# Performance work log

Hardware: AMD Instinct MI355X
Metric: run time of the kernel (lower is better)

The kernel has to match this reference:

```python
import jax, jax.numpy as jnp
import numpy as np

GH, GW = 64, 64     # patch grid
WH, WW = 8, 8       # window size
NH = 8              # num heads
EMB = 128
HD = EMB // NH      # head dim = 16
M = WH * WW         # tokens per window = 64


def _masks():
    # Faithful to the torch code: row_mask blocks cross-shift attention for the
    # last window-row; column_mask is its einops-rearranged counterpart.
    half = WH * (WW // 2)
    row = np.zeros((M, M), np.float32)
    row[-half:, :-half] = -np.inf
    row[:-half, -half:] = -np.inf
    r, c = M // WH, M // WW
    # '(r wh) (c ww) -> (wh r) (ww c)'
    col = row.reshape(r, WH, c, WW).transpose(1, 0, 3, 2).reshape(M, M)
    return jnp.asarray(row), jnp.asarray(col)


def _rel_idx():
    hh, ww_ = np.meshgrid(np.arange(WH), np.arange(WW), indexing='ij')
    coords = np.stack([hh.ravel(), ww_.ravel()], -1)        # (M, 2)
    rel = coords[:, None, :] - coords[None, :, :]           # (M, M, 2)
    return jnp.asarray(rel[..., 0] + WH - 1), jnp.asarray(rel[..., 1] + WW - 1)


def setup_inputs() -> dict:
    key = jax.random.key(0)
    ks = jax.random.split(key, 4)
    B, L = 32, GH * GW
    return {
        'x': jax.random.normal(ks[0], (B, L, EMB), jnp.float32),
        'w1': jax.random.normal(ks[1], (3 * EMB, EMB), jnp.float32) * 0.02,
        'b1': jnp.zeros((3 * EMB,), jnp.float32),
        'w2': jax.random.normal(ks[2], (EMB, EMB), jnp.float32) * 0.02,
        'b2': jnp.zeros((EMB,), jnp.float32),
        'rel_bias': jax.random.normal(ks[3], (2 * WH - 1, 2 * WW - 1), jnp.float32) * 0.02,
    }


def reference(x, w1, b1, w2, b2, rel_bias):
    B, L, C = x.shape
    qkv = x @ w1.T + b1                                   # (B, L, 3C)
    # 'b (h w) (c k) -> b h w c k'  (k=3 varies fastest within channel)
    qkv = qkv.reshape(B, GH, GW, C, 3)
    # cyclic shift by half window
    qkv = jnp.roll(qkv, (-WH // 2, -WW // 2), axis=(1, 2))
    # 'b (Hw wh) (Ww ww) (e H) k -> b H Hw Ww (wh ww) e k'  (head idx fastest in C)
    qkv = qkv.reshape(B, GH // WH, WH, GW // WW, WW, HD, NH, 3)
    qkv = jnp.transpose(qkv, (0, 6, 1, 3, 2, 4, 5, 7))    # b H Hw Ww wh ww e k
    qkv = qkv.reshape(B, NH, GH // WH, GW // WW, M, HD, 3)
    Q, K, V = qkv[..., 0], qkv[..., 1], qkv[..., 2]
    wei = jnp.einsum('bhijqe,bhijke->bhijqk', Q, K) / float(np.sqrt(HD))
    ih, iw = _rel_idx()
    wei = wei + rel_bias[ih, iw]                          # (M, M) bias broadcast
    row_mask, col_mask = _masks()
    wei = wei.at[:, :, -1, :].add(row_mask)               # last window-row
    wei = wei.at[:, :, :, -1].add(col_mask)               # last window-col
    attn = jax.nn.softmax(wei, axis=-1)
    out = jnp.einsum('bhijqk,bhijke->bhijqe', attn, V)    # b H Hw Ww M e
    # 'b H Hw Ww (wh ww) e -> b (Hw wh) (Ww ww) (H e)' then flatten spatial
    out = out.reshape(B, NH, GH // WH, GW // WW, WH, WW, HD)
    out = jnp.transpose(out, (0, 2, 4, 3, 5, 1, 6)).reshape(B, L, C)
    return out @ w2.T + b2
```

## Files before the change

kernel.cpp:

```cpp
#include <hip/hip_runtime.h>
#include <math.h>

typedef _Float16 h4  __attribute__((ext_vector_type(4)));
typedef _Float16 h8  __attribute__((ext_vector_type(8)));
typedef float    f4  __attribute__((ext_vector_type(4)));
typedef float    f32x4 __attribute__((ext_vector_type(4)));

#define W1_ELEMS (384*128)
#define W2_ELEMS (128*128)
#define LOG2E 1.44269504088896340736f

__global__ void cvt_weights(const float* __restrict__ w1, const float* __restrict__ w2,
                            _Float16* __restrict__ w1h, _Float16* __restrict__ w2h) {
    int i = blockIdx.x * 256 + threadIdx.x;
    if (i < W1_ELEMS) {
        int j = i >> 7, k = i & 127;
        int c = j / 3;
        int kind = j - 3 * c;
        int jp = kind * 128 + (c & 7) * 16 + (c >> 3);
        w1h[jp * 128 + k] = (_Float16)w1[i];
    }
    if (i < W2_ELEMS) w2h[i] = (_Float16)w2[i];
}

__global__ __launch_bounds__(512, 4)
void swin_fused(const float* __restrict__ x,
                const float* __restrict__ b1,
                const float* __restrict__ b2,
                const float* __restrict__ rel_bias,
                const _Float16* __restrict__ w1h,
                const _Float16* __restrict__ w2h,
                float* __restrict__ out)
{
    __shared__ _Float16 xh[64*136];
    __shared__ _Float16 QO[8*64*16];
    __shared__ _Float16 Kt[8*64*16];
    __shared__ _Float16 Vt[8*16*68];
    __shared__ _Float16 bm[64*68];

    const int tid  = threadIdx.x;
    const int lane = tid & 63;
    const int wv   = tid >> 6;
    const int quad = lane >> 4;
    const int l16  = lane & 15;
    const int s_lane = (l16 & 3) ^ ((l16 >> 2) & 3);
    const int swz    = (quad ^ s_lane) << 2;

    const int blk = blockIdx.x;
    const int b   = blk >> 6;
    const int Hw  = (blk >> 3) & 7;
    const int Ww  = blk & 7;

    {
        const int r0 = tid >> 5;
        const int c4 = tid & 31;
        #pragma unroll
        for (int it = 0; it < 4; ++it) {
            int t  = r0 + it*16;
            int gi = (Hw*8 + (t >> 3) + 4) & 63;
            int gj = (Ww*8 + (t & 7) + 4) & 63;
            f32x4 v = *(const f32x4*)(x + ((size_t)b*4096 + gi*64 + gj)*128 + c4*4);
            h4 hv;
            hv[0] = (_Float16)v[0]; hv[1] = (_Float16)v[1];
            hv[2] = (_Float16)v[2]; hv[3] = (_Float16)v[3];
            *(h4*)(&xh[t*136 + c4*4]) = hv;
        }
    }
    {
        const int rowm = (Hw == 7);
        const int colm = (Ww == 7);
        #pragma unroll
        for (int it = 0; it < 8; ++it) {
            int f = tid + it*512;
            int j = f >> 6, i = f & 63;
            int hi = i >> 3, wi = i & 7, hj = j >> 3, wj = j & 7;
            float v = rel_bias[(hi - hj + 7)*15 + (wi - wj + 7)] * LOG2E;
            if (rowm && ((i ^ j) & 32)) v = -INFINITY;
            if (colm && ((i ^ j) & 4))  v = -INFINITY;
            bm[i*68 + j] = (_Float16)v;
        }
    }

    float biasv[3][4];
    #pragma unroll
    for (int cc = 0; cc < 3; ++cc)
        #pragma unroll
        for (int r = 0; r < 4; ++r)
            biasv[cc][r] = b1[96*quad + 24*r + 3*wv + cc];

    __syncthreads();

    _Float16* Qh = &QO[wv*1024];
    _Float16* Kh = &Kt[wv*1024];

    {
        f4 acc[3][4];
        #pragma unroll
        for (int cc = 0; cc < 3; ++cc)
            #pragma unroll
            for (int tt = 0; tt < 4; ++tt)
                acc[cc][tt] = (f4){0.f,0.f,0.f,0.f};

        for (int kb = 0; kb < 4; ++kb) {
            h8 bfx[4];
            #pragma unroll
            for (int tt = 0; tt < 4; ++tt)
                bfx[tt] = *(const h8*)(&xh[(tt*16 + l16)*136 + kb*32 + quad*8]);
            #pragma unroll
            for (int cc = 0; cc < 3; ++cc) {
                h8 afw = *(const h8*)(w1h + (size_t)((cc*8 + wv)*16 + l16)*128 + kb*32 + quad*8);
                #pragma unroll
                for (int tt = 0; tt < 4; ++tt)
                    acc[cc][tt] = __builtin_amdgcn_mfma_f32_16x16x32_f16(afw, bfx[tt], acc[cc][tt], 0, 0, 0);
            }
        }

        const float qsc = 0.25f * LOG2E;
        #pragma unroll
        for (int tt = 0; tt < 4; ++tt) {
            int t = tt*16 + l16;
            h4 qv, kv;
            #pragma unroll
            for (int r = 0; r < 4; ++r) {
                qv[r] = (_Float16)((acc[0][tt][r] + biasv[0][r]) * qsc);
                kv[r] = (_Float16)( acc[1][tt][r] + biasv[1][r]);
            }
            *(h4*)(Qh + t*16 + swz) = qv;
            *(h4*)(Kh + t*16 + swz) = kv;
            #pragma unroll
            for (int r = 0; r < 4; ++r)
                Vt[(wv*16 + quad*4 + r)*68 + t] = (_Float16)(acc[2][tt][r] + biasv[2][r]);
        }
    }

    {
        const _Float16* Vh = &Vt[wv*16*68];

        h4 ak[4];
        #pragma unroll
        for (int mt = 0; mt < 4; ++mt)
            ak[mt] = *(const h4*)(Kh + (mt*16 + l16)*16 + swz);
        h4 av[4];
        #pragma unroll
        for (int kt = 0; kt < 4; ++kt)
            av[kt] = *(const h4*)(Vh + l16*68 + kt*16 + quad*4);

        for (int nt = 0; nt < 4; ++nt) {
            h4 bq = *(const h4*)(Qh + (nt*16 + l16)*16 + swz);

            f4 T[4];
            #pragma unroll
            for (int mt = 0; mt < 4; ++mt) {
                f4 z = {0.f,0.f,0.f,0.f};
                T[mt] = __builtin_amdgcn_mfma_f32_16x16x16f16(ak[mt], bq, z, 0, 0, 0);
            }
            #pragma unroll
            for (int mt = 0; mt < 4; ++mt) {
                h4 bmv = *(const h4*)(&bm[(nt*16 + l16)*68 + mt*16 + quad*4]);
                #pragma unroll
                for (int r = 0; r < 4; ++r)
                    T[mt][r] += (float)bmv[r];
            }

            float m = -INFINITY;
            #pragma unroll
            for (int mt = 0; mt < 4; ++mt)
                #pragma unroll
                for (int r = 0; r < 4; ++r) m = fmaxf(m, T[mt][r]);
            m = fmaxf(m, __shfl_xor(m, 16, 64));
            m = fmaxf(m, __shfl_xor(m, 32, 64));
            float s = 0.f;
            h4 P[4];
            #pragma unroll
            for (int mt = 0; mt < 4; ++mt)
                #pragma unroll
                for (int r = 0; r < 4; ++r) {
                    float p = __builtin_amdgcn_exp2f(T[mt][r] - m);
                    s += p;
                    P[mt][r] = (_Float16)p;
                }
            s += __shfl_xor(s, 16, 64);
            s += __shfl_xor(s, 32, 64);
            float rcp = 1.0f / s;

            f4 o = {0.f,0.f,0.f,0.f};
            #pragma unroll
            for (int kt = 0; kt < 4; ++kt)
                o = __builtin_amdgcn_mfma_f32_16x16x16f16(av[kt], P[kt], o, 0, 0, 0);
            h4 ov;
            #pragma unroll
            for (int r = 0; r < 4; ++r) ov[r] = (_Float16)(o[r] * rcp);
            *(h4*)(Qh + (nt*16 + l16)*16 + swz) = ov;
        }
    }
    __syncthreads();

    {
        const int o = wv*16 + l16;
        const int g0 = (quad & 1) * 2;
        const int off0 = ((g0    ) ^ s_lane) << 2;
        const int off1 = ((g0 + 1) ^ s_lane) << 2;

        f4 acc3[4] = {{0.f,0.f,0.f,0.f},{0.f,0.f,0.f,0.f},{0.f,0.f,0.f,0.f},{0.f,0.f,0.f,0.f}};
        for (int kb = 0; kb < 4; ++kb) {
            h8 bf = *(const h8*)(w2h + (size_t)o*128 + kb*32 + quad*8);
            int hh = kb*2 + (quad >> 1);
            #pragma unroll
            for (int mt = 0; mt < 4; ++mt) {
                const _Float16* Ob = &QO[hh*1024 + (mt*16 + l16)*16];
                h4 a0 = *(const h4*)(Ob + off0);
                h4 a1 = *(const h4*)(Ob + off1);
                h8 af = { a0[0], a0[1], a0[2], a0[3], a1[0], a1[1], a1[2], a1[3] };
                acc3[mt] = __builtin_amdgcn_mfma_f32_16x16x32_f16(af, bf, acc3[mt], 0, 0, 0);
            }
        }
        float bias = b2[o];
        #pragma unroll
        for (int mt = 0; mt < 4; ++mt) {
            #pragma unroll
            for (int r = 0; r < 4; ++r) {
                int t  = mt*16 + quad*4 + r;
                int gi = Hw*8 + (t >> 3);
                int gj = Ww*8 + (t & 7);
                out[((size_t)b*4096 + gi*64 + gj)*128 + o] = acc3[mt][r] + bias;
            }
        }
    }
}

extern "C" void kernel_launch(void* const* d_in, const int* in_sizes, int n_in,
                              void* d_out, int out_size, void* d_ws, size_t ws_size,
                              hipStream_t stream) {
    (void)in_sizes; (void)n_in; (void)out_size; (void)ws_size;
    const float* x  = (const float*)d_in[0];
    const float* w1 = (const float*)d_in[1];
    const float* b1 = (const float*)d_in[2];
    const float* w2 = (const float*)d_in[3];
    const float* b2 = (const float*)d_in[4];
    const float* rb = (const float*)d_in[5];

    _Float16* w1h = (_Float16*)d_ws;
    _Float16* w2h = (_Float16*)((char*)d_ws + (size_t)W1_ELEMS * sizeof(_Float16));
    float* outp = (float*)d_out;

    cvt_weights<<<(W1_ELEMS + 255)/256, 256, 0, stream>>>(w1, w2, w1h, w2h);
    swin_fused<<<32*64, 512, 0, stream>>>(x, b1, b2, rb, w1h, w2h, outp);
}
```

Measured before the change: 157.0 us.

## Keep Q/K/V in registers and precompute bias-mask tables in prep kernel

QKV projection results now feed attention straight from MFMA accumulators. V is computed transposed so its fragment layout matches the PV MFMA operand. This removes the Q/K/V shared-memory round trip and its swizzle, and shrinks LDS to two 64x136 buffers. The four bias/mask variants are precomputed once into a global fp16 table by the weight-conversion kernel, replacing per-block rel_bias gathers with global reads of that table. Attention output is written to a row-major LDS tile, and the output-projection operands are loaded once up front. The trade-offs are higher register pressure and bias reads that now come from global memory/cache.

```diff
diff --git a/kernel.cpp b/kernel.cpp
--- a/kernel.cpp
+++ b/kernel.cpp
@@ -8,10 +8,13 @@
 
 #define W1_ELEMS (384*128)
 #define W2_ELEMS (128*128)
+#define BM_ELEMS (4*64*64)
 #define LOG2E 1.44269504088896340736f
 
 __global__ void cvt_weights(const float* __restrict__ w1, const float* __restrict__ w2,
-                            _Float16* __restrict__ w1h, _Float16* __restrict__ w2h) {
+                            const float* __restrict__ rel_bias,
+                            _Float16* __restrict__ w1h, _Float16* __restrict__ w2h,
+                            _Float16* __restrict__ bmg) {
     int i = blockIdx.x * 256 + threadIdx.x;
     if (i < W1_ELEMS) {
         int j = i >> 7, k = i & 127;
@@ -21,30 +24,33 @@
         w1h[jp * 128 + k] = (_Float16)w1[i];
     }
     if (i < W2_ELEMS) w2h[i] = (_Float16)w2[i];
+    if (i < BM_ELEMS) {
+        int v = i >> 12, f = i & 4095;
+        int ti = f >> 6, tj = f & 63;
+        float val = rel_bias[((ti >> 3) - (tj >> 3) + 7) * 15 + ((ti & 7) - (tj & 7) + 7)] * LOG2E;
+        if ((v & 2) && ((ti ^ tj) & 32)) val = -INFINITY;
+        if ((v & 1) && ((ti ^ tj) & 4))  val = -INFINITY;
+        bmg[i] = (_Float16)val;
+    }
 }
 
 __global__ __launch_bounds__(512, 4)
 void swin_fused(const float* __restrict__ x,
                 const float* __restrict__ b1,
                 const float* __restrict__ b2,
-                const float* __restrict__ rel_bias,
                 const _Float16* __restrict__ w1h,
                 const _Float16* __restrict__ w2h,
+                const _Float16* __restrict__ bmg,
                 float* __restrict__ out)
 {
     __shared__ _Float16 xh[64*136];
-    __shared__ _Float16 QO[8*64*16];
-    __shared__ _Float16 Kt[8*64*16];
-    __shared__ _Float16 Vt[8*16*68];
-    __shared__ _Float16 bm[64*68];
+    __shared__ _Float16 Ob[64*136];
 
     const int tid  = threadIdx.x;
     const int lane = tid & 63;
     const int wv   = tid >> 6;
     const int quad = lane >> 4;
     const int l16  = lane & 15;
-    const int s_lane = (l16 & 3) ^ ((l16 >> 2) & 3);
-    const int swz    = (quad ^ s_lane) << 2;
 
     const int blk = blockIdx.x;
     const int b   = blk >> 6;
@@ -66,87 +72,62 @@
             *(h4*)(&xh[t*136 + c4*4]) = hv;
         }
     }
+
+    float bQ[4], bK[4];
+    #pragma unroll
+    for (int r = 0; r < 4; ++r) {
+        bQ[r] = b1[24*(quad*4 + r) + 3*wv + 0];
+        bK[r] = b1[24*(quad*4 + r) + 3*wv + 1];
+    }
+    const float bV = b1[24*l16 + 3*wv + 2];
+
+    __syncthreads();
+
+    f4 accQ[4], accK[4], accV[4];
+    #pragma unroll
+    for (int tt = 0; tt < 4; ++tt) {
+        accQ[tt] = (f4){0.f,0.f,0.f,0.f};
+        accK[tt] = (f4){0.f,0.f,0.f,0.f};
+        accV[tt] = (f4){0.f,0.f,0.f,0.f};
+    }
+    for (int kb = 0; kb < 4; ++kb) {
+        h8 bfx[4];
+        #pragma unroll
+        for (int tt = 0; tt < 4; ++tt)
+            bfx[tt] = *(const h8*)(&xh[(tt*16 + l16)*136 + kb*32 + quad*8]);
+        h8 aQ = *(const h8*)(w1h + (size_t)((0*8 + wv)*16 + l16)*128 + kb*32 + quad*8);
+        h8 aK = *(const h8*)(w1h + (size_t)((1*8 + wv)*16 + l16)*128 + kb*32 + quad*8);
+        h8 aV = *(const h8*)(w1h + (size_t)((2*8 + wv)*16 + l16)*128 + kb*32 + quad*8);
+        #pragma unroll
+        for (int tt = 0; tt < 4; ++tt) {
+            accQ[tt] = __builtin_amdgcn_mfma_f32_16x16x32_f16(aQ, bfx[tt], accQ[tt], 0, 0, 0);
+            accK[tt] = __builtin_amdgcn_mfma_f32_16x16x32_f16(aK, bfx[tt], accK[tt], 0, 0, 0);
+            accV[tt] = __builtin_amdgcn_mfma_f32_16x16x32_f16(bfx[tt], aV, accV[tt], 0, 0, 0);
+        }
+    }
+
     {
-        const int rowm = (Hw == 7);
-        const int colm = (Ww == 7);
-        #pragma unroll
-        for (int it = 0; it < 8; ++it) {
-            int f = tid + it*512;
-            int j = f >> 6, i = f & 63;
-            int hi = i >> 3, wi = i & 7, hj = j >> 3, wj = j & 7;
-            float v = rel_bias[(hi - hj + 7)*15 + (wi - wj + 7)] * LOG2E;
-            if (rowm && ((i ^ j) & 32)) v = -INFINITY;
-            if (colm && ((i ^ j) & 4))  v = -INFINITY;
-            bm[i*68 + j] = (_Float16)v;
-        }
-    }
-
-    float biasv[3][4];
-    #pragma unroll
-    for (int cc = 0; cc < 3; ++cc)
-        #pragma unroll
-        for (int r = 0; r < 4; ++r)
-            biasv[cc][r] = b1[96*quad + 24*r + 3*wv + cc];
-
-    __syncthreads();
-
-    _Float16* Qh = &QO[wv*1024];
-    _Float16* Kh = &Kt[wv*1024];
-
-    {
-        f4 acc[3][4];
-        #pragma unroll
-        for (int cc = 0; cc < 3; ++cc)
-            #pragma unroll
-            for (int tt = 0; tt < 4; ++tt)
-                acc[cc][tt] = (f4){0.f,0.f,0.f,0.f};
-
-        for (int kb = 0; kb < 4; ++kb) {
-            h8 bfx[4];
-            #pragma unroll
-            for (int tt = 0; tt < 4; ++tt)
-                bfx[tt] = *(const h8*)(&xh[(tt*16 + l16)*136 + kb*32 + quad*8]);
-            #pragma unroll
-            for (int cc = 0; cc < 3; ++cc) {
-                h8 afw = *(const h8*)(w1h + (size_t)((cc*8 + wv)*16 + l16)*128 + kb*32 + quad*8);
-                #pragma unroll
-                for (int tt = 0; tt < 4; ++tt)
-                    acc[cc][tt] = __builtin_amdgcn_mfma_f32_16x16x32_f16(afw, bfx[tt], acc[cc][tt], 0, 0, 0);
-            }
-        }
-
+        const _Float16* bmp = bmg + ((((Hw == 7) ? 2 : 0) | ((Ww == 7) ? 1 : 0)) << 12);
         const float qsc = 0.25f * LOG2E;
-        #pragma unroll
-        for (int tt = 0; tt < 4; ++tt) {
-            int t = tt*16 + l16;
-            h4 qv, kv;
-            #pragma unroll
-            for (int r = 0; r < 4; ++r) {
-                qv[r] = (_Float16)((acc[0][tt][r] + biasv[0][r]) * qsc);
-                kv[r] = (_Float16)( acc[1][tt][r] + biasv[1][r]);
-            }
-            *(h4*)(Qh + t*16 + swz) = qv;
-            *(h4*)(Kh + t*16 + swz) = kv;
+
+        h4 ak[4];
+        #pragma unroll
+        for (int mt = 0; mt < 4; ++mt)
             #pragma unroll
             for (int r = 0; r < 4; ++r)
-                Vt[(wv*16 + quad*4 + r)*68 + t] = (_Float16)(acc[2][tt][r] + biasv[2][r]);
-        }
-    }
-
-    {
-        const _Float16* Vh = &Vt[wv*16*68];
-
-        h4 ak[4];
-        #pragma unroll
-        for (int mt = 0; mt < 4; ++mt)
-            ak[mt] = *(const h4*)(Kh + (mt*16 + l16)*16 + swz);
+                ak[mt][r] = (_Float16)(accK[mt][r] + bK[r]);
         h4 av[4];
         #pragma unroll
         for (int kt = 0; kt < 4; ++kt)
-            av[kt] = *(const h4*)(Vh + l16*68 + kt*16 + quad*4);
+            #pragma unroll
+            for (int r = 0; r < 4; ++r)
+                av[kt][r] = (_Float16)(accV[kt][r] + bV);
 
         for (int nt = 0; nt < 4; ++nt) {
-            h4 bq = *(const h4*)(Qh + (nt*16 + l16)*16 + swz);
+            h4 bq;
+            #pragma unroll
+            for (int i = 0; i < 4; ++i)
+                bq[i] = (_Float16)((accQ[nt][i] + bQ[i]) * qsc);
 
             f4 T[4];
             #pragma unroll
@@ -156,7 +137,7 @@
             }
             #pragma unroll
             for (int mt = 0; mt < 4; ++mt) {
-                h4 bmv = *(const h4*)(&bm[(nt*16 + l16)*68 + mt*16 + quad*4]);
+                h4 bmv = *(const h4*)(bmp + (nt*16 + l16)*64 + mt*16 + quad*4);
                 #pragma unroll
                 for (int r = 0; r < 4; ++r)
                     T[mt][r] += (float)bmv[r];
@@ -190,29 +171,26 @@
             h4 ov;
             #pragma unroll
             for (int r = 0; r < 4; ++r) ov[r] = (_Float16)(o[r] * rcp);
-            *(h4*)(Qh + (nt*16 + l16)*16 + swz) = ov;
+            *(h4*)(&Ob[(nt*16 + l16)*136 + wv*16 + quad*4]) = ov;
         }
     }
     __syncthreads();
 
     {
+        h8 af[4][4];
+        #pragma unroll
+        for (int mt = 0; mt < 4; ++mt)
+            #pragma unroll
+            for (int kb = 0; kb < 4; ++kb)
+                af[mt][kb] = *(const h8*)(&Ob[(mt*16 + l16)*136 + kb*32 + quad*8]);
+
         const int o = wv*16 + l16;
-        const int g0 = (quad & 1) * 2;
-        const int off0 = ((g0    ) ^ s_lane) << 2;
-        const int off1 = ((g0 + 1) ^ s_lane) << 2;
-
         f4 acc3[4] = {{0.f,0.f,0.f,0.f},{0.f,0.f,0.f,0.f},{0.f,0.f,0.f,0.f},{0.f,0.f,0.f,0.f}};
         for (int kb = 0; kb < 4; ++kb) {
             h8 bf = *(const h8*)(w2h + (size_t)o*128 + kb*32 + quad*8);
-            int hh = kb*2 + (quad >> 1);
-            #pragma unroll
-            for (int mt = 0; mt < 4; ++mt) {
-                const _Float16* Ob = &QO[hh*1024 + (mt*16 + l16)*16];
-                h4 a0 = *(const h4*)(Ob + off0);
-                h4 a1 = *(const h4*)(Ob + off1);
-                h8 af = { a0[0], a0[1], a0[2], a0[3], a1[0], a1[1], a1[2], a1[3] };
-                acc3[mt] = __builtin_amdgcn_mfma_f32_16x16x32_f16(af, bf, acc3[mt], 0, 0, 0);
-            }
+            #pragma unroll
+            for (int mt = 0; mt < 4; ++mt)
+                acc3[mt] = __builtin_amdgcn_mfma_f32_16x16x32_f16(af[mt][kb], bf, acc3[mt], 0, 0, 0);
         }
         float bias = b2[o];
         #pragma unroll
@@ -241,8 +219,9 @@
 
     _Float16* w1h = (_Float16*)d_ws;
     _Float16* w2h = (_Float16*)((char*)d_ws + (size_t)W1_ELEMS * sizeof(_Float16));
+    _Float16* bmg = (_Float16*)((char*)d_ws + (size_t)(W1_ELEMS + W2_ELEMS) * sizeof(_Float16));
     float* outp = (float*)d_out;
 
-    cvt_weights<<<(W1_ELEMS + 255)/256, 256, 0, stream>>>(w1, w2, w1h, w2h);
-    swin_fused<<<32*64, 512, 0, stream>>>(x, b1, b2, rb, w1h, w2h, outp);
+    cvt_weights<<<(W1_ELEMS + 255)/256, 256, 0, stream>>>(w1, w2, rb, w1h, w2h, bmg);
+    swin_fused<<<32*64, 512, 0, stream>>>(x, b1, b2, w1h, w2h, bmg, outp);
 }
```

Result: slower. 175.2 us (+11.6%).
